# Optimization experiments

Measured on AMD Instinct MI355X. Metric: run time of the kernel, lower is better.

The kernel has to match this reference:

```python
import jax, jax.numpy as jnp
import numpy as np

B, IN, E, H, V, T = 512, 256, 256, 512, 32000, 32


def setup_inputs() -> dict:
    key = jax.random.key(0)
    ks = jax.random.split(key, 8)
    s = 0.05
    return {
        "x": jax.random.normal(ks[0], (B, IN), jnp.float32),
        "agent_w": jax.random.normal(ks[1], (H, IN), jnp.float32) * s,
        "agent_b": jnp.zeros((H,), jnp.float32),
        "sos": jax.random.normal(ks[2], (E,), jnp.float32) * 0.01,
        "emb": jax.random.normal(ks[3], (V, E), jnp.float32) * s,
        "W_ih": jax.random.normal(ks[4], (3 * H, E), jnp.float32) * s,
        "W_hh": jax.random.normal(ks[5], (3 * H, H), jnp.float32) * s,
        "b_ih": jnp.zeros((3 * H,), jnp.float32),
        "b_hh": jnp.zeros((3 * H,), jnp.float32),
        "W_out": jax.random.normal(ks[6], (V, H), jnp.float32) * s,
        "b_out": jnp.zeros((V,), jnp.float32),
        "W_stop": jax.random.normal(ks[7], (1, H), jnp.float32) * s,
        "b_stop": jnp.zeros((1,), jnp.float32),
    }


def _gru_cell(inp, h, W_ih, W_hh, b_ih, b_hh):
    gi = inp @ W_ih.T + b_ih              # [B, 3H]
    gh = h @ W_hh.T + b_hh                # [B, 3H]
    i_r, i_z, i_n = jnp.split(gi, 3, axis=1)
    h_r, h_z, h_n = jnp.split(gh, 3, axis=1)
    r = jax.nn.sigmoid(i_r + h_r)
    z = jax.nn.sigmoid(i_z + h_z)
    n = jnp.tanh(i_n + r * h_n)
    return (1.0 - z) * n + z * h


def reference(x, agent_w, agent_b, sos, emb, W_ih, W_hh, b_ih, b_hh,
              W_out, b_out, W_stop, b_stop):
    h0 = x @ agent_w.T + agent_b                       # agent(x) -> [B, H]
    inp0 = jnp.broadcast_to(sos, (x.shape[0], sos.shape[0]))
    keys = jax.random.split(jax.random.key(42), T)

    def step(carry, k):
        h, inp = carry
        h = _gru_cell(inp, h, W_ih, W_hh, b_ih, b_hh)  # noise_scale=0 -> no noise
        symb_logits = h @ W_out.T + b_out              # [B, V]
        stop_logit = (h @ W_stop.T + b_stop)[:, 0]     # [B]
        logp = jax.nn.log_softmax(symb_logits, axis=1)
        k1, k2 = jax.random.split(k)
        symb = jax.random.categorical(k1, symb_logits, axis=1)          # [B] int
        p_stop = jax.nn.sigmoid(stop_logit)
        stop = jax.random.bernoulli(k2, p_stop).astype(jnp.float32)     # [B]
        symb_lp = jnp.take_along_axis(logp, symb[:, None], axis=1)[:, 0]
        # Bernoulli: log p = s - softplus(s), log(1-p) = -softplus(s)
        sp = jax.nn.softplus(stop_logit)
        stop_lp = stop * stop_logit - sp
        symb_ent = -jnp.sum(jnp.exp(logp) * logp, axis=1)
        stop_ent = sp - stop_logit * p_stop
        inp_next = emb[symb]
        return (h, inp_next), (symb, stop, symb_lp, stop_lp, symb_ent, stop_ent)

    _, ys = jax.lax.scan(step, (h0, inp0), keys)
    symb_seq, stop_seq, symb_lp, stop_lp, symb_ent, stop_ent = ys
    # [T, B] -> [B, T]
    tr = lambda a: a.T
    return (tr(symb_seq), tr(stop_seq).astype(jnp.int32),
            tr(symb_lp), tr(stop_lp), tr(symb_ent), tr(stop_ent))
```

## Files before the change

### kernel.cpp

```cpp
#include <hip/hip_runtime.h>
#include <hip/hip_bf16.h>
#include <stdint.h>

#define JAX_PARTITIONABLE 1

#define Bz 512
#define INz 256
#define Ez 256
#define Hz 512
#define Vz 32000
#define Tz 32
#define BTz (Bz * Tz)
#define TINYF 1.17549435e-38f

typedef float otype;
__device__ __forceinline__ void store_out(otype* out, int idx, float v) {
  out[idx] = v;
}

__device__ __forceinline__ uint32_t rotl32(uint32_t x, int r) {
  return (x << r) | (x >> (32 - r));
}
__device__ __forceinline__ void threefry2x32(uint32_t k0, uint32_t k1,
                                             uint32_t x0, uint32_t x1,
                                             uint32_t& o0, uint32_t& o1) {
  const uint32_t ks2 = k0 ^ k1 ^ 0x1BD11BDAu;
  x0 += k0; x1 += k1;
#define TF_R4(a, b, c, d)                              \
  x0 += x1; x1 = rotl32(x1, a); x1 ^= x0;              \
  x0 += x1; x1 = rotl32(x1, b); x1 ^= x0;              \
  x0 += x1; x1 = rotl32(x1, c); x1 ^= x0;              \
  x0 += x1; x1 = rotl32(x1, d); x1 ^= x0;
  TF_R4(13, 15, 26, 6)  x0 += k1;  x1 += ks2 + 1u;
  TF_R4(17, 29, 16, 24) x0 += ks2; x1 += k0 + 2u;
  TF_R4(13, 15, 26, 6)  x0 += k0;  x1 += k1 + 3u;
  TF_R4(17, 29, 16, 24) x0 += k1;  x1 += ks2 + 4u;
  TF_R4(13, 15, 26, 6)  x0 += ks2; x1 += k0 + 5u;
#undef TF_R4
  o0 = x0; o1 = x1;
}
__device__ __forceinline__ uint32_t rand_bits32(uint32_t ka, uint32_t kb,
                                                uint32_t idx, uint32_t n) {
#if JAX_PARTITIONABLE
  (void)n;
  uint32_t o0, o1;
  threefry2x32(ka, kb, 0u, idx, o0, o1);
  return o0 ^ o1;
#else
  uint32_t half = n >> 1;
  uint32_t o0, o1;
  if (idx < half) { threefry2x32(ka, kb, idx, idx + half, o0, o1); return o0; }
  threefry2x32(ka, kb, idx - half, idx, o0, o1); return o1;
#endif
}
__device__ __forceinline__ float bits_to_f01(uint32_t bits) {
  return __uint_as_float((bits >> 9) | 0x3f800000u) - 1.0f;
}

__global__ void RnnSenderReinforce_36799279792759_kernel(otype* __restrict__ out,
                                                         int n, float v) {
  int i = blockIdx.x * 256 + threadIdx.x;
  if (i < n) out[i] = v;
}

__global__ void keys_kernel(uint32_t* __restrict__ keys) {
  int t = threadIdx.x;
  if (t >= Tz) return;
  uint32_t ka, kb;
#if JAX_PARTITIONABLE
  threefry2x32(0u, 42u, 0u, (uint32_t)t, ka, kb);
#else
  {
    uint32_t j0 = 2u * t, j1 = 2u * t + 1u;
    uint32_t a0, a1, b0, b1;
    if (j0 < Tz) { threefry2x32(0u, 42u, j0, j0 + Tz, a0, a1); ka = a0; }
    else         { threefry2x32(0u, 42u, j0 - Tz, j0, a0, a1); ka = a1; }
    if (j1 < Tz) { threefry2x32(0u, 42u, j1, j1 + Tz, b0, b1); kb = b0; }
    else         { threefry2x32(0u, 42u, j1 - Tz, j1, b0, b1); kb = b1; }
  }
#endif
  uint32_t o0, o1;
#if JAX_PARTITIONABLE
  threefry2x32(ka, kb, 0u, 0u, o0, o1);
  keys[t * 4 + 0] = o0; keys[t * 4 + 1] = o1;
  threefry2x32(ka, kb, 0u, 1u, o0, o1);
  keys[t * 4 + 2] = o0; keys[t * 4 + 3] = o1;
#else
  uint32_t p0, p1, q0, q1;
  threefry2x32(ka, kb, 0u, 2u, p0, p1);
  threefry2x32(ka, kb, 1u, 3u, q0, q1);
  keys[t * 4 + 0] = p0; keys[t * 4 + 1] = q0;
  keys[t * 4 + 2] = p1; keys[t * 4 + 3] = q1;
#endif
}

#define GBM 64
#define GBN 64
#define GBK 32
#define LDSS 68

__device__ __forceinline__ void gemm_bt_body(const float* __restrict__ A,
                                             const float* __restrict__ W,
                                             const float* __restrict__ bias,
                                             float* __restrict__ C,
                                             int M, int N, int K,
                                             int bx, int by,
                                             float* As, float* Bs) {
  const int tid = threadIdx.x;
  const int tx = tid & 15;
  const int ty = tid >> 4;
  const int m0 = by * GBM;
  const int n0 = bx * GBN;
  const int lr = tid >> 3;
  const int lc = (tid & 7) << 2;

  float acc[4][4] = {};
  const float* Ap = A + (size_t)(m0 + lr) * K + lc;
  const float* Wp = W + (size_t)(n0 + lr) * K + lc;
  const size_t rstep = (size_t)32 * K;

  for (int k0 = 0; k0 < K; k0 += GBK) {
    float4 a0 = *(const float4*)(Ap + k0);
    float4 a1 = *(const float4*)(Ap + k0 + rstep);
    float4 b0 = *(const float4*)(Wp + k0);
    float4 b1 = *(const float4*)(Wp + k0 + rstep);
    __syncthreads();
    As[(lc + 0) * LDSS + lr] = a0.x;
    As[(lc + 1) * LDSS + lr] = a0.y;
    As[(lc + 2) * LDSS + lr] = a0.z;
    As[(lc + 3) * LDSS + lr] = a0.w;
    As[(lc + 0) * LDSS + lr + 32] = a1.x;
    As[(lc + 1) * LDSS + lr + 32] = a1.y;
    As[(lc + 2) * LDSS + lr + 32] = a1.z;
    As[(lc + 3) * LDSS + lr + 32] = a1.w;
    Bs[(lc + 0) * LDSS + lr] = b0.x;
    Bs[(lc + 1) * LDSS + lr] = b0.y;
    Bs[(lc + 2) * LDSS + lr] = b0.z;
    Bs[(lc + 3) * LDSS + lr] = b0.w;
    Bs[(lc + 0) * LDSS + lr + 32] = b1.x;
    Bs[(lc + 1) * LDSS + lr + 32] = b1.y;
    Bs[(lc + 2) * LDSS + lr + 32] = b1.z;
    Bs[(lc + 3) * LDSS + lr + 32] = b1.w;
    __syncthreads();
#pragma unroll
    for (int kk = 0; kk < GBK; kk++) {
      float4 af = *(const float4*)&As[kk * LDSS + (ty << 2)];
      float4 bf = *(const float4*)&Bs[kk * LDSS + (tx << 2)];
      float ar[4] = {af.x, af.y, af.z, af.w};
      float br[4] = {bf.x, bf.y, bf.z, bf.w};
#pragma unroll
      for (int i = 0; i < 4; i++)
#pragma unroll
        for (int j = 0; j < 4; j++)
          acc[i][j] = fmaf(ar[i], br[j], acc[i][j]);
    }
  }

  const int nc = n0 + (tx << 2);
  float4 bv;
  bv.x = bias[nc + 0]; bv.y = bias[nc + 1]; bv.z = bias[nc + 2]; bv.w = bias[nc + 3];
#pragma unroll
  for (int i = 0; i < 4; i++) {
    int m = m0 + (ty << 2) + i;
    float4 o;
    o.x = acc[i][0] + bv.x;
    o.y = acc[i][1] + bv.y;
    o.z = acc[i][2] + bv.z;
    o.w = acc[i][3] + bv.w;
    *(float4*)(C + (size_t)m * N + nc) = o;
  }
}

__global__ __launch_bounds__(256) void gemm_bt(const float* __restrict__ A,
                                               const float* __restrict__ W,
                                               const float* __restrict__ bias,
                                               float* __restrict__ C,
                                               int M, int N, int K) {
  __shared__ __align__(16) float As[GBK * LDSS];
  __shared__ __align__(16) float Bs[GBK * LDSS];
  gemm_bt_body(A, W, bias, C, M, N, K, blockIdx.x, blockIdx.y, As, Bs);
}

__global__ __launch_bounds__(256) void gru2_kernel(const float* __restrict__ inp,
                                                   const float* __restrict__ Wih,
                                                   const float* __restrict__ bih,
                                                   float* __restrict__ gi,
                                                   const float* __restrict__ h,
                                                   const float* __restrict__ Whh,
                                                   const float* __restrict__ bhh,
                                                   float* __restrict__ gh) {
  __shared__ __align__(16) float As[GBK * LDSS];
  __shared__ __align__(16) float Bs[GBK * LDSS];
  if (blockIdx.z == 0)
    gemm_bt_body(inp, Wih, bih, gi, Bz, 3 * Hz, Ez, blockIdx.x, blockIdx.y, As, Bs);
  else
    gemm_bt_body(h, Whh, bhh, gh, Bz, 3 * Hz, Hz, blockIdx.x, blockIdx.y, As, Bs);
}

#define QBM 256
#define QBN 128
#define QBK 32
#define QLDA 260
#define QLDB 132

__global__ __launch_bounds__(512, 4) void gemm256_bt(const float* __restrict__ A,
                                                     const float* __restrict__ W,
                                                     const float* __restrict__ bias,
                                                     float* __restrict__ C,
                                                     int M, int N, int K) {
  __shared__ __align__(16) float As[QBK * QLDA];
  __shared__ __align__(16) float Bs[QBK * QLDB];
  const int tid = threadIdx.x;
  const int tx = tid & 15;
  const int ty = tid >> 4;

  const int nP = N / QBN;
  const int G = nP >> 3;
  const int lim = G << 4;
  int b = blockIdx.x;
  int P, mi;
  if (b < lim) {
    int g = b >> 4, r = b & 15;
    mi = r >> 3;
    P = (g << 3) + (r & 7);
  } else {
    int e = b - lim;
    P = (G << 3) + (e & 1);
    mi = e >> 1;
  }
  const int m0 = mi * QBM;
  const int n0 = P * QBN;

  const int ar = tid >> 1;
  const int ak = (tid & 1) << 4;
  const int br = tid >> 2;
  const int bk = (tid & 3) << 2;

  const float* Ap = A + (size_t)(m0 + ar) * K + ak;
  const float* Wp = W + (size_t)(n0 + br) * K + bk;

  float4 a0 = *(const float4*)(Ap);
  float4 a1 = *(const float4*)(Ap + 4);
  float4 a2 = *(const float4*)(Ap + 8);
  float4 a3 = *(const float4*)(Ap + 12);
  float4 b0 = *(const float4*)(Wp);
  float4 b1 = *(const float4*)(Wp + 16);

  float acc[8][8] = {};

  for (int k0 = 0; k0 < K; k0 += QBK) {
    __syncthreads();
    As[(ak + 0) * QLDA + ar] = a0.x;
    As[(ak + 1) * QLDA + ar] = a0.y;
    As[(ak + 2) * QLDA + ar] = a0.z;
    As[(ak + 3) * QLDA + ar] = a0.w;
    As[(ak + 4) * QLDA + ar] = a1.x;
    As[(ak + 5) * QLDA + ar] = a1.y;
    As[(ak + 6) * QLDA + ar] = a1.z;
    As[(ak + 7) * QLDA + ar] = a1.w;
    As[(ak + 8) * QLDA + ar] = a2.x;
    As[(ak + 9) * QLDA + ar] = a2.y;
    As[(ak + 10) * QLDA + ar] = a2.z;
    As[(ak + 11) * QLDA + ar] = a2.w;
    As[(ak + 12) * QLDA + ar] = a3.x;
    As[(ak + 13) * QLDA + ar] = a3.y;
    As[(ak + 14) * QLDA + ar] = a3.z;
    As[(ak + 15) * QLDA + ar] = a3.w;
    Bs[(bk + 0) * QLDB + br] = b0.x;
    Bs[(bk + 1) * QLDB + br] = b0.y;
    Bs[(bk + 2) * QLDB + br] = b0.z;
    Bs[(bk + 3) * QLDB + br] = b0.w;
    Bs[(16 + bk + 0) * QLDB + br] = b1.x;
    Bs[(16 + bk + 1) * QLDB + br] = b1.y;
    Bs[(16 + bk + 2) * QLDB + br] = b1.z;
    Bs[(16 + bk + 3) * QLDB + br] = b1.w;
    __syncthreads();
    if (k0 + QBK < K) {
      a0 = *(const float4*)(Ap + k0 + QBK);
      a1 = *(const float4*)(Ap + k0 + QBK + 4);
      a2 = *(const float4*)(Ap + k0 + QBK + 8);
      a3 = *(const float4*)(Ap + k0 + QBK + 12);
      b0 = *(const float4*)(Wp + k0 + QBK);
      b1 = *(const float4*)(Wp + k0 + QBK + 16);
    }
#pragma unroll 4
    for (int kk = 0; kk < QBK; kk++) {
      float4 xa0 = *(const float4*)&As[kk * QLDA + (ty << 2)];
      float4 xa1 = *(const float4*)&As[kk * QLDA + 128 + (ty << 2)];
      float4 xb0 = *(const float4*)&Bs[kk * QLDB + (tx << 2)];
      float4 xb1 = *(const float4*)&Bs[kk * QLDB + 64 + (tx << 2)];
      float ar8[8] = {xa0.x, xa0.y, xa0.z, xa0.w, xa1.x, xa1.y, xa1.z, xa1.w};
      float br8[8] = {xb0.x, xb0.y, xb0.z, xb0.w, xb1.x, xb1.y, xb1.z, xb1.w};
#pragma unroll
      for (int i = 0; i < 8; i++)
#pragma unroll
        for (int j = 0; j < 8; j++)
          acc[i][j] = fmaf(ar8[i], br8[j], acc[i][j]);
    }
  }

  const int nc0 = n0 + (tx << 2);
  const float4 bv0 = *(const float4*)(bias + nc0);
  const float4 bv1 = *(const float4*)(bias + nc0 + 64);
#pragma unroll
  for (int hf = 0; hf < 2; hf++) {
#pragma unroll
    for (int i = 0; i < 4; i++) {
      const int m = m0 + hf * 128 + (ty << 2) + i;
      float* Cp = C + (size_t)m * N + nc0;
      float4 o;
      o.x = acc[hf * 4 + i][0] + bv0.x;
      o.y = acc[hf * 4 + i][1] + bv0.y;
      o.z = acc[hf * 4 + i][2] + bv0.z;
      o.w = acc[hf * 4 + i][3] + bv0.w;
      *(float4*)Cp = o;
      float4 o2;
      o2.x = acc[hf * 4 + i][4] + bv1.x;
      o2.y = acc[hf * 4 + i][5] + bv1.y;
      o2.z = acc[hf * 4 + i][6] + bv1.z;
      o2.w = acc[hf * 4 + i][7] + bv1.w;
      *(float4*)(Cp + 64) = o2;
    }
  }
}

__global__ void gates_kernel(const float* __restrict__ gi,
                             const float* __restrict__ gh,
                             float* __restrict__ h) {
  int idx = blockIdx.x * 256 + threadIdx.x;
  int b = idx >> 9;
  int j = idx & 511;
  const float* gib = gi + (size_t)b * (3 * Hz);
  const float* ghb = gh + (size_t)b * (3 * Hz);
  float ir = gib[j], iz = gib[j + Hz], in_ = gib[j + 2 * Hz];
  float hr = ghb[j], hz = ghb[j + Hz], hn = ghb[j + 2 * Hz];
  float r = 1.0f / (1.0f + expf(-(ir + hr)));
  float z = 1.0f / (1.0f + expf(-(iz + hz)));
  float n = tanhf(in_ + r * hn);
  float hv = h[idx];
  h[idx] = (1.0f - z) * n + z * hv;
}

__global__ __launch_bounds__(256) void stop_kernel(const float* __restrict__ h,
                                                   const float* __restrict__ W_stop,
                                                   const float* __restrict__ b_stop,
                                                   const uint32_t* __restrict__ keys,
                                                   int t, otype* __restrict__ out) {
  int wave = threadIdx.x >> 6;
  int lane = threadIdx.x & 63;
  int b = blockIdx.x * 4 + wave;
  const float* hb = h + (size_t)b * Hz;
  float s = 0.0f;
  for (int k = lane; k < Hz; k += 64) s = fmaf(hb[k], W_stop[k], s);
#pragma unroll
  for (int off = 32; off; off >>= 1) s += __shfl_down(s, off, 64);
  if (lane == 0) {
    s += b_stop[0];
    uint32_t bits = rand_bits32(keys[t * 4 + 2], keys[t * 4 + 3], (uint32_t)b, Bz);
    float u = bits_to_f01(bits);
    float p = 1.0f / (1.0f + expf(-s));
    float stop = (u < p) ? 1.0f : 0.0f;
    float sp = fmaxf(s, 0.0f) + log1pf(expf(-fabsf(s)));
    store_out(out, 1 * BTz + b * Tz + t, stop);
    store_out(out, 3 * BTz + b * Tz + t, stop * s - sp);
    store_out(out, 5 * BTz + b * Tz + t, sp - s * p);
  }
}

__global__ __launch_bounds__(256) void sample_kernel(const float* __restrict__ logits,
                                                     const uint32_t* __restrict__ keys,
                                                     int t, otype* __restrict__ out,
                                                     int* __restrict__ symb_i) {
  __shared__ float sm[256], sg[256], sgl[256], sz[256], ss[256];
  __shared__ int sgi[256];
  const int tid = threadIdx.x;
  const int b = blockIdx.x;
  const float* lb = logits + (size_t)b * Vz;
  const uint32_t k1a = keys[t * 4 + 0], k1b = keys[t * 4 + 1];
  const uint32_t base = (uint32_t)b * (uint32_t)Vz;

  float m = -INFINITY, gbest = -INFINITY, glogit = 0.0f;
  int gidx = 0x7FFFFFFF;
  for (int v = tid; v < Vz; v += 256) {
    float l = lb[v];
    m = fmaxf(m, l);
    uint32_t bits = rand_bits32(k1a, k1b, base + (uint32_t)v, (uint32_t)Bz * Vz);
    float f = bits_to_f01(bits);
    float u = fmaxf(TINYF, f + TINYF);
    float g = -logf(-logf(u));
    float val = l + g;
    if (val > gbest) { gbest = val; gidx = v; glogit = l; }
  }
  sm[tid] = m; sg[tid] = gbest; sgi[tid] = gidx; sgl[tid] = glogit;
  __syncthreads();
  for (int s2 = 128; s2; s2 >>= 1) {
    if (tid < s2) {
      sm[tid] = fmaxf(sm[tid], sm[tid + s2]);
      float go = sg[tid + s2]; int io = sgi[tid + s2];
      if (go > sg[tid] || (go == sg[tid] && io < sgi[tid])) {
        sg[tid] = go; sgi[tid] = io; sgl[tid] = sgl[tid + s2];
      }
    }
    __syncthreads();
  }
  const float M = sm[0];

  float Z = 0.0f, S1 = 0.0f;
  for (int v = tid; v < Vz; v += 256) {
    float sft = lb[v] - M;
    float e = expf(sft);
    Z += e;
    S1 = fmaf(e, sft, S1);
  }
  sz[tid] = Z; ss[tid] = S1;
  __syncthreads();
  for (int s2 = 128; s2; s2 >>= 1) {
    if (tid < s2) { sz[tid] += sz[tid + s2]; ss[tid] += ss[tid + s2]; }
    __syncthreads();
  }
  if (tid == 0) {
    float Zt = sz[0], S1t = ss[0];
    float lse = logf(Zt);
    int symb = sgi[0];
    store_out(out, 0 * BTz + b * Tz + t, (float)symb);
    store_out(out, 2 * BTz + b * Tz + t, (sgl[0] - M) - lse);
    store_out(out, 4 * BTz + b * Tz + t, lse - S1t / Zt);
    symb_i[b] = symb;
  }
}

__global__ void init_inp_kernel(float* __restrict__ inp, const float* __restrict__ sos) {
  inp[blockIdx.x * Ez + threadIdx.x] = sos[threadIdx.x];
}
__global__ void gather_kernel(const float* __restrict__ emb,
                              const int* __restrict__ symb_i,
                              float* __restrict__ inp) {
  int b = blockIdx.x;
  int s = symb_i[b];
  s = (s < 0) ? 0 : ((s >= Vz) ? (Vz - 1) : s);
  inp[(size_t)b * Ez + threadIdx.x] = emb[(size_t)s * Ez + threadIdx.x];
}

extern "C" __attribute__((visibility("default")))
void kernel_launch(void* const* d_in, const int* in_sizes, int n_in,
                   void* d_out, int out_size, void* d_ws, size_t ws_size,
                   hipStream_t stream) {
  const float* x       = (const float*)d_in[0];
  const float* agent_w = (const float*)d_in[1];
  const float* agent_b = (const float*)d_in[2];
  const float* sos     = (const float*)d_in[3];
  const float* emb     = (const float*)d_in[4];
  const float* W_ih    = (const float*)d_in[5];
  const float* W_hh    = (const float*)d_in[6];
  const float* b_ih    = (const float*)d_in[7];
  const float* b_hh    = (const float*)d_in[8];
  const float* W_out   = (const float*)d_in[9];
  const float* b_out   = (const float*)d_in[10];
  const float* W_stop  = (const float*)d_in[11];
  const float* b_stop  = (const float*)d_in[12];
  otype* out = (otype*)d_out;

  float* ws = (float*)d_ws;
  float* h      = ws;
  float* inp    = h + (size_t)Bz * Hz;
  float* gi     = inp + (size_t)Bz * Ez;
  float* gh     = gi + (size_t)Bz * 3 * Hz;
  float* logits = gh + (size_t)Bz * 3 * Hz;
  int* symb_i   = (int*)(logits + (size_t)Bz * Vz);
  uint32_t* keys = (uint32_t*)(symb_i + Bz);

  keys_kernel<<<1, 64, 0, stream>>>(keys);
  init_inp_kernel<<<Bz, Ez, 0, stream>>>(inp, sos);
  gemm_bt<<<dim3(Hz / GBN, Bz / GBM), 256, 0, stream>>>(x, agent_w, agent_b, h,
                                                        Bz, Hz, INz);
  for (int t = 0; t < Tz; t++) {
    gru2_kernel<<<dim3(3 * Hz / GBN, Bz / GBM, 2), 256, 0, stream>>>(
        inp, W_ih, b_ih, gi, h, W_hh, b_hh, gh);
    gates_kernel<<<(Bz * Hz) / 256, 256, 0, stream>>>(gi, gh, h);
    gemm256_bt<<<(Vz / QBN) * (Bz / QBM), 512, 0, stream>>>(h, W_out, b_out,
                                                            logits, Bz, Vz, Hz);
    stop_kernel<<<Bz / 4, 256, 0, stream>>>(h, W_stop, b_stop, keys, t, out);
    sample_kernel<<<Bz, 256, 0, stream>>>(logits, keys, t, out, symb_i);
    gather_kernel<<<Bz, Ez, 0, stream>>>(emb, symb_i, inp);
  }
}
```

Before: 10.82 ms.

## Fuse stop head into gates kernel, gather into sampler, widen sampler to 1024 threads

Merges the GRU gate update with the stop-logit dot product and Bernoulli sampling, using one block per batch row with the new hidden state staged in shared memory. Folds the embedding gather into the sampling kernel through a shared symbol. Raises the sampler's block size to 1024 threads so the Gumbel-max pass (threefry plus two logs per vocab entry) is spread over four sub-groups, then combines their partial results. Each step now launches two fewer kernels, at the cost of larger blocks and idle threads during the softmax-sum pass.

```diff
diff --git a/kernel.cpp b/kernel.cpp
--- a/kernel.cpp
+++ b/kernel.cpp
@@ -324,12 +324,14 @@
   }
 }
 
-__global__ void gates_kernel(const float* __restrict__ gi,
-                             const float* __restrict__ gh,
-                             float* __restrict__ h) {
-  int idx = blockIdx.x * 256 + threadIdx.x;
-  int b = idx >> 9;
-  int j = idx & 511;
+__global__ __launch_bounds__(512) void gates_stop_kernel(
+    const float* __restrict__ gi, const float* __restrict__ gh,
+    float* __restrict__ h, const float* __restrict__ W_stop,
+    const float* __restrict__ b_stop, const uint32_t* __restrict__ keys,
+    int t, otype* __restrict__ out) {
+  __shared__ float hrow[Hz];
+  const int b = blockIdx.x;
+  const int j = threadIdx.x;
   const float* gib = gi + (size_t)b * (3 * Hz);
   const float* ghb = gh + (size_t)b * (3 * Hz);
   float ir = gib[j], iz = gib[j + Hz], in_ = gib[j + 2 * Hz];
@@ -337,43 +339,44 @@
   float r = 1.0f / (1.0f + expf(-(ir + hr)));
   float z = 1.0f / (1.0f + expf(-(iz + hz)));
   float n = tanhf(in_ + r * hn);
-  float hv = h[idx];
-  h[idx] = (1.0f - z) * n + z * hv;
-}
-
-__global__ __launch_bounds__(256) void stop_kernel(const float* __restrict__ h,
-                                                   const float* __restrict__ W_stop,
-                                                   const float* __restrict__ b_stop,
-                                                   const uint32_t* __restrict__ keys,
-                                                   int t, otype* __restrict__ out) {
-  int wave = threadIdx.x >> 6;
-  int lane = threadIdx.x & 63;
-  int b = blockIdx.x * 4 + wave;
-  const float* hb = h + (size_t)b * Hz;
-  float s = 0.0f;
-  for (int k = lane; k < Hz; k += 64) s = fmaf(hb[k], W_stop[k], s);
-#pragma unroll
-  for (int off = 32; off; off >>= 1) s += __shfl_down(s, off, 64);
-  if (lane == 0) {
-    s += b_stop[0];
-    uint32_t bits = rand_bits32(keys[t * 4 + 2], keys[t * 4 + 3], (uint32_t)b, Bz);
-    float u = bits_to_f01(bits);
-    float p = 1.0f / (1.0f + expf(-s));
-    float stop = (u < p) ? 1.0f : 0.0f;
-    float sp = fmaxf(s, 0.0f) + log1pf(expf(-fabsf(s)));
-    store_out(out, 1 * BTz + b * Tz + t, stop);
-    store_out(out, 3 * BTz + b * Tz + t, stop * s - sp);
-    store_out(out, 5 * BTz + b * Tz + t, sp - s * p);
-  }
-}
-
-__global__ __launch_bounds__(256) void sample_kernel(const float* __restrict__ logits,
-                                                     const uint32_t* __restrict__ keys,
-                                                     int t, otype* __restrict__ out,
-                                                     int* __restrict__ symb_i) {
+  float hv = h[(size_t)b * Hz + j];
+  float hnew = (1.0f - z) * n + z * hv;
+  h[(size_t)b * Hz + j] = hnew;
+  hrow[j] = hnew;
+  __syncthreads();
+  if (j < 64) {
+    const int lane = j;
+    float s = 0.0f;
+    for (int k = lane; k < Hz; k += 64) s = fmaf(hrow[k], W_stop[k], s);
+#pragma unroll
+    for (int off = 32; off; off >>= 1) s += __shfl_down(s, off, 64);
+    if (lane == 0) {
+      s += b_stop[0];
+      uint32_t bits = rand_bits32(keys[t * 4 + 2], keys[t * 4 + 3], (uint32_t)b, Bz);
+      float u = bits_to_f01(bits);
+      float p = 1.0f / (1.0f + expf(-s));
+      float stop = (u < p) ? 1.0f : 0.0f;
+      float sp = fmaxf(s, 0.0f) + log1pf(expf(-fabsf(s)));
+      store_out(out, 1 * BTz + b * Tz + t, stop);
+      store_out(out, 3 * BTz + b * Tz + t, stop * s - sp);
+      store_out(out, 5 * BTz + b * Tz + t, sp - s * p);
+    }
+  }
+}
+
+__global__ __launch_bounds__(1024) void sample_kernel(const float* __restrict__ logits,
+                                                      const uint32_t* __restrict__ keys,
+                                                      int t, otype* __restrict__ out,
+                                                      const float* __restrict__ emb,
+                                                      float* __restrict__ inp) {
+  __shared__ float sm4[1024], sg4[1024], sgl4[1024];
+  __shared__ int sgi4[1024];
   __shared__ float sm[256], sg[256], sgl[256], sz[256], ss[256];
   __shared__ int sgi[256];
-  const int tid = threadIdx.x;
+  __shared__ int ssymb;
+  const int tid4 = threadIdx.x;
+  const int tid = tid4 & 255;
+  const int sub = tid4 >> 8;
   const int b = blockIdx.x;
   const float* lb = logits + (size_t)b * Vz;
   const uint32_t k1a = keys[t * 4 + 0], k1b = keys[t * 4 + 1];
@@ -381,7 +384,7 @@
 
   float m = -INFINITY, gbest = -INFINITY, glogit = 0.0f;
   int gidx = 0x7FFFFFFF;
-  for (int v = tid; v < Vz; v += 256) {
+  for (int v = tid + (sub << 8); v < Vz; v += 1024) {
     float l = lb[v];
     m = fmaxf(m, l);
     uint32_t bits = rand_bits32(k1a, k1b, base + (uint32_t)v, (uint32_t)Bz * Vz);
@@ -391,54 +394,67 @@
     float val = l + g;
     if (val > gbest) { gbest = val; gidx = v; glogit = l; }
   }
-  sm[tid] = m; sg[tid] = gbest; sgi[tid] = gidx; sgl[tid] = glogit;
+  sm4[tid4] = m; sg4[tid4] = gbest; sgi4[tid4] = gidx; sgl4[tid4] = glogit;
+  __syncthreads();
+  if (tid4 < 256) {
+#pragma unroll
+    for (int s4 = 1; s4 < 4; s4++) {
+      int o = tid4 + (s4 << 8);
+      m = fmaxf(m, sm4[o]);
+      float go = sg4[o]; int io = sgi4[o];
+      if (go > gbest || (go == gbest && io < gidx)) {
+        gbest = go; gidx = io; glogit = sgl4[o];
+      }
+    }
+    sm[tid4] = m; sg[tid4] = gbest; sgi[tid4] = gidx; sgl[tid4] = glogit;
+  }
   __syncthreads();
   for (int s2 = 128; s2; s2 >>= 1) {
-    if (tid < s2) {
-      sm[tid] = fmaxf(sm[tid], sm[tid + s2]);
-      float go = sg[tid + s2]; int io = sgi[tid + s2];
-      if (go > sg[tid] || (go == sg[tid] && io < sgi[tid])) {
-        sg[tid] = go; sgi[tid] = io; sgl[tid] = sgl[tid + s2];
+    if (tid4 < s2) {
+      sm[tid4] = fmaxf(sm[tid4], sm[tid4 + s2]);
+      float go = sg[tid4 + s2]; int io = sgi[tid4 + s2];
+      if (go > sg[tid4] || (go == sg[tid4] && io < sgi[tid4])) {
+        sg[tid4] = go; sgi[tid4] = io; sgl[tid4] = sgl[tid4 + s2];
       }
     }
     __syncthreads();
   }
   const float M = sm[0];
 
-  float Z = 0.0f, S1 = 0.0f;
-  for (int v = tid; v < Vz; v += 256) {
-    float sft = lb[v] - M;
-    float e = expf(sft);
-    Z += e;
-    S1 = fmaf(e, sft, S1);
-  }
-  sz[tid] = Z; ss[tid] = S1;
+  if (tid4 < 256) {
+    float Z = 0.0f, S1 = 0.0f;
+    for (int v = tid4; v < Vz; v += 256) {
+      float sft = lb[v] - M;
+      float e = expf(sft);
+      Z += e;
+      S1 = fmaf(e, sft, S1);
+    }
+    sz[tid4] = Z; ss[tid4] = S1;
+  }
   __syncthreads();
   for (int s2 = 128; s2; s2 >>= 1) {
-    if (tid < s2) { sz[tid] += sz[tid + s2]; ss[tid] += ss[tid + s2]; }
+    if (tid4 < s2) { sz[tid4] += sz[tid4 + s2]; ss[tid4] += ss[tid4 + s2]; }
     __syncthreads();
   }
-  if (tid == 0) {
+  if (tid4 == 0) {
     float Zt = sz[0], S1t = ss[0];
     float lse = logf(Zt);
     int symb = sgi[0];
     store_out(out, 0 * BTz + b * Tz + t, (float)symb);
     store_out(out, 2 * BTz + b * Tz + t, (sgl[0] - M) - lse);
     store_out(out, 4 * BTz + b * Tz + t, lse - S1t / Zt);
-    symb_i[b] = symb;
+    ssymb = symb;
+  }
+  __syncthreads();
+  if (tid4 < Ez) {
+    int s = ssymb;
+    s = (s < 0) ? 0 : ((s >= Vz) ? (Vz - 1) : s);
+    inp[(size_t)b * Ez + tid4] = emb[(size_t)s * Ez + tid4];
   }
 }
 
 __global__ void init_inp_kernel(float* __restrict__ inp, const float* __restrict__ sos) {
   inp[blockIdx.x * Ez + threadIdx.x] = sos[threadIdx.x];
-}
-__global__ void gather_kernel(const float* __restrict__ emb,
-                              const int* __restrict__ symb_i,
-                              float* __restrict__ inp) {
-  int b = blockIdx.x;
-  int s = symb_i[b];
-  s = (s < 0) ? 0 : ((s >= Vz) ? (Vz - 1) : s);
-  inp[(size_t)b * Ez + threadIdx.x] = emb[(size_t)s * Ez + threadIdx.x];
 }
 
 extern "C" __attribute__((visibility("default")))
@@ -466,8 +482,7 @@
   float* gi     = inp + (size_t)Bz * Ez;
   float* gh     = gi + (size_t)Bz * 3 * Hz;
   float* logits = gh + (size_t)Bz * 3 * Hz;
-  int* symb_i   = (int*)(logits + (size_t)Bz * Vz);
-  uint32_t* keys = (uint32_t*)(symb_i + Bz);
+  uint32_t* keys = (uint32_t*)(logits + (size_t)Bz * Vz);
 
   keys_kernel<<<1, 64, 0, stream>>>(keys);
   init_inp_kernel<<<Bz, Ez, 0, stream>>>(inp, sos);
@@ -476,11 +491,10 @@
   for (int t = 0; t < Tz; t++) {
     gru2_kernel<<<dim3(3 * Hz / GBN, Bz / GBM, 2), 256, 0, stream>>>(
         inp, W_ih, b_ih, gi, h, W_hh, b_hh, gh);
-    gates_kernel<<<(Bz * Hz) / 256, 256, 0, stream>>>(gi, gh, h);
+    gates_stop_kernel<<<Bz, 512, 0, stream>>>(gi, gh, h, W_stop, b_stop, keys,
+                                              t, out);
     gemm256_bt<<<(Vz / QBN) * (Bz / QBM), 512, 0, stream>>>(h, W_out, b_out,
                                                             logits, Bz, Vz, Hz);
-    stop_kernel<<<Bz / 4, 256, 0, stream>>>(h, W_stop, b_stop, keys, t, out);
-    sample_kernel<<<Bz, 256, 0, stream>>>(logits, keys, t, out, symb_i);
-    gather_kernel<<<Bz, Ez, 0, stream>>>(emb, symb_i, inp);
-  }
-}
+    sample_kernel<<<Bz, 1024, 0, stream>>>(logits, keys, t, out, emb, inp);
+  }
+}
```

Measured after the change: 10.45 ms (median of 2 runs). 3.4% less time.
